# Optimization experiments

Hardware: AMD Instinct MI355X
Metric: run time of the kernel (lower is better)

## Reference

```python
import jax, jax.numpy as jnp
import numpy as np

EMB_DIM = 1024
NUM_HEADS = 16
HEAD_DIM = EMB_DIM // NUM_HEADS  # 64
B, S = 2, 2048


def setup_inputs() -> dict:
    key = jax.random.key(0)
    ks = jax.random.split(key, 9)
    scale = 1.0 / np.sqrt(EMB_DIM)
    return {
        "query": jax.random.normal(ks[0], (B, S, EMB_DIM), dtype=jnp.float32),
        "Wq": jax.random.normal(ks[1], (EMB_DIM, EMB_DIM), dtype=jnp.float32) * scale,
        "bq": jax.random.normal(ks[2], (EMB_DIM,), dtype=jnp.float32) * 0.01,
        "Wk": jax.random.normal(ks[3], (EMB_DIM, EMB_DIM), dtype=jnp.float32) * scale,
        "bk": jax.random.normal(ks[4], (EMB_DIM,), dtype=jnp.float32) * 0.01,
        "Wv": jax.random.normal(ks[5], (EMB_DIM, EMB_DIM), dtype=jnp.float32) * scale,
        "bv": jax.random.normal(ks[6], (EMB_DIM,), dtype=jnp.float32) * 0.01,
        "Wo": jax.random.normal(ks[7], (EMB_DIM, EMB_DIM), dtype=jnp.float32) * scale,
        "bo": jax.random.normal(ks[8], (EMB_DIM,), dtype=jnp.float32) * 0.01,
    }


def reference(query, Wq, bq, Wk, bk, Wv, bv, Wo, bo):
    # Self-attention path (key_value=None, mask=None in the original forward).
    b, s, _ = query.shape
    # torch nn.Linear: y = x @ W.T + b
    def proj(x, W, bias):
        y = jnp.einsum('bse,fe->bsf', x, W) + bias
        # [B,S,E] -> [B,H,S,D]
        return y.reshape(b, s, NUM_HEADS, HEAD_DIM).transpose(0, 2, 1, 3)

    q = proj(query, Wq, bq)
    k = proj(query, Wk, bk)
    v = proj(query, Wv, bv)

    scores = jnp.einsum('bhqd,bhkd->bhqk', q, k) / np.sqrt(HEAD_DIM).astype(np.float32)
    attn = jax.nn.softmax(scores, axis=-1)  # [B,H,S,S]
    out = jnp.einsum('bhqk,bhkd->bhqd', attn, v)
    out = out.transpose(0, 2, 1, 3).reshape(b, s, EMB_DIM)
    return jnp.einsum('bse,fe->bsf', out, Wo) + bo
```

## Files before the change

### kernel.cpp

```cpp
#include <hip/hip_runtime.h>
#include <hip/hip_bf16.h>

using bf16x4 = __attribute__((ext_vector_type(4))) short;
using short8 = __attribute__((ext_vector_type(8))) short;
using f32x4  = __attribute__((ext_vector_type(4))) float;
using f32x16 = __attribute__((ext_vector_type(16))) float;
using u32x2  = __attribute__((ext_vector_type(2))) unsigned;

__device__ __forceinline__ short f2bf(float f) {
  unsigned u = __builtin_bit_cast(unsigned, f);
  u = (u + 0x7fffu + ((u >> 16) & 1u)) >> 16;
  return (short)u;
}
__device__ __forceinline__ unsigned pk2(float a, float b) {
  __hip_bfloat162 h = __float22bfloat162_rn(make_float2(a, b));
  unsigned u; __builtin_memcpy(&u, &h, 4);
  return u;
}
__device__ __forceinline__ void gload16(const short* g, short* l) {
  __builtin_amdgcn_global_load_lds(
      (const __attribute__((address_space(1))) unsigned int*)g,
      (__attribute__((address_space(3))) unsigned int*)l, 16, 0, 0);
}
__device__ __forceinline__ void pl32swap(unsigned &a, unsigned &b) {
  asm("v_permlane32_swap_b32 %0, %1" : "+v"(a), "+v"(b));
}

constexpr int E  = 1024;
constexpr int SL = 2048;
constexpr int NB = 2;
constexpr int NH = 16;
constexpr int M  = NB * SL;

__global__ __launch_bounds__(256) void convert_kernel(
    const float* __restrict__ X,  const float* __restrict__ Wq,
    const float* __restrict__ Wk, const float* __restrict__ Wv,
    const float* __restrict__ Wo, short* __restrict__ out)
{
  const size_t i8 = ((size_t)blockIdx.x * 256 + threadIdx.x) * 8;
  const float* src;
  if (i8 < (size_t)(4u << 20)) {
    src = X + i8;
  } else {
    size_t r = i8 - (size_t)(4u << 20);
    int wi = (int)(r >> 20);
    size_t off = r & ((1u << 20) - 1);
    src = (wi == 0 ? Wq : wi == 1 ? Wk : wi == 2 ? Wv : Wo) + off;
  }
  f32x4 a = *(const f32x4*)src;
  f32x4 b = *(const f32x4*)(src + 4);
  short hb[8];
#pragma unroll
  for (int e = 0; e < 4; ++e) { hb[e] = f2bf(a[e]); hb[4 + e] = f2bf(b[e]); }
  *(short8*)(out + i8) = *(short8*)hb;
}

template <bool OUTF32, bool PROJ>
__device__ __forceinline__ void gemm_body(
    const short* __restrict__ A0, const short* __restrict__ A1, const short* __restrict__ A2,
    const short* __restrict__ B0, const short* __restrict__ B1, const short* __restrict__ B2,
    const float* __restrict__ b0, const float* __restrict__ b1, const float* __restrict__ b2,
    void* __restrict__ Y0, void* __restrict__ Y1, void* __restrict__ Y2,
    float s0, float s1, float s2, int ld0, int ld1, int ld2)
{
  constexpr int BK = 32;
  constexpr int TM = 128, TN = 128;
  constexpr int RA = TM / 64;
  constexpr int RB = TN / 64;
  constexpr int WM = TM / 2, WN = TN / 2;
  constexpr int NI = WM / 16, NJ = WN / 16;
  __shared__ alignas(16) short As[2][TM * BK];
  __shared__ alignas(16) short Bs[2][TN * BK];
  const int t = threadIdx.x;
  const int l = t & 63;
  const int w = t >> 6;
  const int c = l & 15;
  const int g = l >> 4;

  const int fid = (int)blockIdx.x;
  int z, m0, n0;
  if (PROJ) {
    const int orig = (fid & 7) * 96 + (fid >> 3);
    z = orig >> 8;
    const int rem = orig & 255;
    const bool sw = (z != 2);
    m0 = (sw ? (rem >> 5) : (rem & 31)) * TM;
    n0 = (sw ? (rem & 31) : (rem >> 5)) * TN;
  } else {
    const int orig = (fid & 7) * 32 + (fid >> 3);
    z = 0;
    m0 = (orig & 7) * TM;
    n0 = (orig >> 3) * TN;
  }
  const short* Ap = (z == 0) ? A0 : (z == 1) ? A1 : A2;
  const short* Bp = (z == 0) ? B0 : (z == 1) ? B1 : B2;
  const float* bp = (z == 0) ? b0 : (z == 1) ? b1 : b2;
  void* Yp        = (z == 0) ? Y0 : (z == 1) ? Y1 : Y2;
  const float sc  = (z == 0) ? s0 : (z == 1) ? s1 : s2;
  const int ldY   = (z == 0) ? ld0 : (z == 1) ? ld1 : ld2;
  const bool swp  = PROJ ? (z != 2) : true;

  const short* gA[RA]; int oA[RA];
  const short* gB[RB]; int oB[RB];
#pragma unroll
  for (int r = 0; r < RA; ++r) {
    const int cc = r * 256 + t;
    gA[r] = Ap + (size_t)(m0 + (cc >> 2)) * E + (cc & 3) * 8;
    oA[r] = (r * 256 + (t & ~63)) * 8;
  }
#pragma unroll
  for (int r = 0; r < RB; ++r) {
    const int cc = r * 256 + t;
    gB[r] = Bp + (size_t)(n0 + (cc >> 2)) * E + (cc & 3) * 8;
    oB[r] = (r * 256 + (t & ~63)) * 8;
  }

#pragma unroll
  for (int r = 0; r < RA; ++r) gload16(gA[r], &As[0][oA[r]]);
#pragma unroll
  for (int r = 0; r < RB; ++r) gload16(gB[r], &Bs[0][oB[r]]);

  const int wm = (w >> 1) * WM;
  const int wn = (w & 1) * WN;
  f32x4 acc[NI][NJ] = {};
  int cur = 0;

  for (int k0 = 0; k0 < E; k0 += BK) {
    __syncthreads();
    if (k0 + BK < E) {
#pragma unroll
      for (int r = 0; r < RA; ++r) gload16(gA[r] + k0 + BK, &As[cur ^ 1][oA[r]]);
#pragma unroll
      for (int r = 0; r < RB; ++r) gload16(gB[r] + k0 + BK, &Bs[cur ^ 1][oB[r]]);
    }
    short8 ah[NI], bfr[NJ];
#pragma unroll
    for (int i = 0; i < NI; ++i)
      ah[i] = *(const short8*)&As[cur][(wm + i * 16 + c) * BK + g * 8];
#pragma unroll
    for (int j = 0; j < NJ; ++j)
      bfr[j] = *(const short8*)&Bs[cur][(wn + j * 16 + c) * BK + g * 8];
#pragma unroll
    for (int i = 0; i < NI; ++i)
#pragma unroll
      for (int j = 0; j < NJ; ++j)
        acc[i][j] = __builtin_amdgcn_mfma_f32_16x16x32_bf16(ah[i], bfr[j], acc[i][j], 0, 0, 0);
    cur ^= 1;
  }

  float bm[NI][4];
  if (swp) {
#pragma unroll
    for (int i = 0; i < NI; ++i)
#pragma unroll
      for (int r = 0; r < 4; ++r)
        bm[i][r] = bp[m0 + wm + i * 16 + g * 4 + r];
  }
#pragma unroll
  for (int j = 0; j < NJ; ++j) {
    const int col = n0 + wn + j * 16 + c;
    const float bj = swp ? 0.f : bp[col];
#pragma unroll
    for (int i = 0; i < NI; ++i) {
      const int row = m0 + wm + i * 16 + g * 4;
      float v[4];
#pragma unroll
      for (int r = 0; r < 4; ++r)
        v[r] = (acc[i][j][r] + (swp ? bm[i][r] : bj)) * sc;
      if (OUTF32) {
        f32x4 o = {v[0], v[1], v[2], v[3]};
        *(f32x4*)((float*)Yp + (size_t)col * ldY + row) = o;
      } else {
        u32x2 o = {pk2(v[0], v[1]), pk2(v[2], v[3])};
        *(u32x2*)((short*)Yp + (size_t)col * ldY + row) = o;
      }
    }
  }
}

__global__ __launch_bounds__(256) void proj_kernel(
    const short* A0, const short* A1, const short* A2,
    const short* B0, const short* B1, const short* B2,
    const float* b0, const float* b1, const float* b2,
    void* Y0, void* Y1, void* Y2,
    float s0, float s1, float s2, int ld0, int ld1, int ld2)
{
  gemm_body<false, true>(A0, A1, A2, B0, B1, B2, b0, b1, b2,
                         Y0, Y1, Y2, s0, s1, s2, ld0, ld1, ld2);
}

__global__ __launch_bounds__(256) void out_kernel(
    const short* A0, const short* A1, const short* A2,
    const short* B0, const short* B1, const short* B2,
    const float* b0, const float* b1, const float* b2,
    void* Y0, void* Y1, void* Y2,
    float s0, float s1, float s2, int ld0, int ld1, int ld2)
{
  gemm_body<true, false>(A0, A1, A2, B0, B1, B2, b0, b1, b2,
                         Y0, Y1, Y2, s0, s1, s2, ld0, ld1, ld2);
}

__global__ __launch_bounds__(512, 2) void flash_kernel(
    const short* __restrict__ Qm, const short* __restrict__ Km,
    const short* __restrict__ VTm, short* __restrict__ Oh)
{
  __shared__ alignas(16) short Ks[2][64][64];
  __shared__ alignas(16) short Vt[2][64][64];
  const int t = threadIdx.x;
  const int l = t & 63;
  const int w = t >> 6;
  const int c = l & 31;
  const int hi = l >> 5;
  const int fid = (int)blockIdx.x;
  const int orig = (fid & 7) * 32 + (fid >> 3);
  const int q0 = (orig & 7) * 256;
  const int bh = orig >> 3;
  const int bat = bh >> 4;
  const int h = bh & 15;
  const size_t baseK = (size_t)bat * SL * E + h * 64;
  const size_t baseV = (size_t)(h * 64) * M + (size_t)bat * SL;

  short8 qf[4];
  {
    const short* qp = Qm + baseK + (size_t)(q0 + w * 32 + c) * E + hi * 8;
#pragma unroll
    for (int tt = 0; tt < 4; ++tt) qf[tt] = *(const short8*)(qp + tt * 16);
  }

  const int sr = t >> 3, sg = t & 7;
  const int swz = (sg ^ (sr & 7)) * 8;
  const short* gK0 = Km + baseK + (size_t)sr * E + sg * 8;
  const short* gV0 = VTm + baseV + (size_t)sr * M + sg * 8;
  const int wo0 = sr * 64 + swz;

  short8 k0r, v0r;
  k0r = *(const short8*)gK0;
  v0r = *(const short8*)gV0;
  *(short8*)(&Ks[0][0][0] + wo0) = k0r;
  *(short8*)(&Vt[0][0][0] + wo0) = v0r;
  k0r = *(const short8*)(gK0 + (size_t)64 * E);
  v0r = *(const short8*)(gV0 + 64);

  f32x16 oa0 = {}, oa1 = {};
  f32x4 lacc = {0.f, 0.f, 0.f, 0.f};
  __syncthreads();

  constexpr int NTT = SL / 64;
  const int sx = c & 7;
  for (int kt = 0; kt < NTT; ++kt) {
    const int cur = kt & 1;
    if (kt + 1 < NTT) {
      *(short8*)(&Ks[cur ^ 1][0][0] + wo0) = k0r;
      *(short8*)(&Vt[cur ^ 1][0][0] + wo0) = v0r;
      if (kt + 2 < NTT) {
        k0r = *(const short8*)(gK0 + (size_t)(kt + 2) * 64 * E);
        v0r = *(const short8*)(gV0 + (kt + 2) * 64);
      }
    }
    const short* Kc0 = &Ks[cur][c][0];
    const short* Kc1 = &Ks[cur][32 + c][0];
    const short* Vc0 = &Vt[cur][c][0];
    const short* Vc1 = &Vt[cur][32 + c][0];

    f32x16 st0 = {}, st1 = {};
    __builtin_amdgcn_s_setprio(1);
#pragma unroll
    for (int tt = 0; tt < 4; ++tt) {
      const int off = ((tt * 2 + hi) ^ sx) * 8;
      short8 kf0 = *(const short8*)(Kc0 + off);
      short8 kf1 = *(const short8*)(Kc1 + off);
      st0 = __builtin_amdgcn_mfma_f32_32x32x16_bf16(kf0, qf[tt], st0, 0, 0, 0);
      st1 = __builtin_amdgcn_mfma_f32_32x32x16_bf16(kf1, qf[tt], st1, 0, 0, 0);
    }
    __builtin_amdgcn_s_setprio(0);

    float p0[16], p1[16];
#pragma unroll
    for (int i = 0; i < 16; ++i) p0[i] = __builtin_amdgcn_exp2f(st0[i]);
#pragma unroll
    for (int i = 0; i < 16; ++i) p1[i] = __builtin_amdgcn_exp2f(st1[i]);
#pragma unroll
    for (int i = 0; i < 16; ++i) lacc[i & 3] += p0[i] + p1[i];

    unsigned W0[4][2], W1[4][2];
#pragma unroll
    for (int b8 = 0; b8 < 4; ++b8) {
      W0[b8][0] = pk2(p0[4 * b8 + 0], p0[4 * b8 + 1]);
      W0[b8][1] = pk2(p0[4 * b8 + 2], p0[4 * b8 + 3]);
      W1[b8][0] = pk2(p1[4 * b8 + 0], p1[4 * b8 + 1]);
      W1[b8][1] = pk2(p1[4 * b8 + 2], p1[4 * b8 + 3]);
    }

    __builtin_amdgcn_s_setprio(1);
#pragma unroll
    for (int tt = 0; tt < 4; ++tt) {
      unsigned a0, a1, b0, b1;
      if (tt == 0)      { a0 = W0[0][0]; a1 = W0[0][1]; b0 = W0[1][0]; b1 = W0[1][1]; }
      else if (tt == 1) { a0 = W0[2][0]; a1 = W0[2][1]; b0 = W0[3][0]; b1 = W0[3][1]; }
      else if (tt == 2) { a0 = W1[0][0]; a1 = W1[0][1]; b0 = W1[1][0]; b1 = W1[1][1]; }
      else              { a0 = W1[2][0]; a1 = W1[2][1]; b0 = W1[3][0]; b1 = W1[3][1]; }
      pl32swap(a0, b0);
      pl32swap(a1, b1);
      union { unsigned u[4]; short8 s8; } pf;
      pf.u[0] = a0; pf.u[1] = a1; pf.u[2] = b0; pf.u[3] = b1;
      const int off = ((tt * 2 + hi) ^ sx) * 8;
      short8 vf0 = *(const short8*)(Vc0 + off);
      short8 vf1 = *(const short8*)(Vc1 + off);
      oa0 = __builtin_amdgcn_mfma_f32_32x32x16_bf16(vf0, pf.s8, oa0, 0, 0, 0);
      oa1 = __builtin_amdgcn_mfma_f32_32x32x16_bf16(vf1, pf.s8, oa1, 0, 0, 0);
    }
    __builtin_amdgcn_s_setprio(0);
    __syncthreads();
  }

  float s = lacc[0] + lacc[1] + lacc[2] + lacc[3];
  s += __shfl_xor(s, 32);
  const float inv = 1.0f / s;
  const int q = q0 + w * 32 + c;
  short* op = Oh + ((size_t)bat * SL + q) * E + h * 64 + hi * 4;
#pragma unroll
  for (int b8 = 0; b8 < 4; ++b8) {
    u32x2 t0 = {pk2(oa0[4 * b8 + 0] * inv, oa0[4 * b8 + 1] * inv),
                pk2(oa0[4 * b8 + 2] * inv, oa0[4 * b8 + 3] * inv)};
    *(u32x2*)(op + b8 * 8) = t0;
    u32x2 t1 = {pk2(oa1[4 * b8 + 0] * inv, oa1[4 * b8 + 1] * inv),
                pk2(oa1[4 * b8 + 2] * inv, oa1[4 * b8 + 3] * inv)};
    *(u32x2*)(op + 32 + b8 * 8) = t1;
  }
}

extern "C" void kernel_launch(void* const* d_in, const int* in_sizes, int n_in,
                              void* d_out, int out_size, void* d_ws, size_t ws_size,
                              hipStream_t stream)
{
  const float* X  = (const float*)d_in[0];
  const float* Wq = (const float*)d_in[1];
  const float* bq = (const float*)d_in[2];
  const float* Wk = (const float*)d_in[3];
  const float* bk = (const float*)d_in[4];
  const float* Wv = (const float*)d_in[5];
  const float* bv = (const float*)d_in[6];
  const float* Wo = (const float*)d_in[7];
  const float* bo = (const float*)d_in[8];
  float* out = (float*)d_out;

  const size_t szX = (size_t)M * E;
  const size_t szW = (size_t)E * E;
  short* Xb  = (short*)d_ws;
  short* Wqb = Xb + szX;
  short* Wkb = Wqb + szW;
  short* Wvb = Wkb + szW;
  short* Wob = Wvb + szW;
  short* Qw  = Wob + szW;
  short* Kw  = Qw + szX;
  short* VTw = Kw + szX;

  convert_kernel<<<4096, 256, 0, stream>>>(X, Wq, Wk, Wv, Wo, Xb);

  const float kLog2eOver8 = 0.18033688011112042f;
  proj_kernel<<<768, 256, 0, stream>>>(
      Wqb, Wkb, Xb,
      Xb, Xb, Wvb,
      bq, bk, bv,
      (void*)Qw, (void*)Kw, (void*)VTw,
      kLog2eOver8, 1.0f, 1.0f, E, E, M);

  flash_kernel<<<256, 512, 0, stream>>>(Qw, Kw, VTw, Qw );

  out_kernel<<<256, 256, 0, stream>>>(
      Wob, Wob, Wob,
      Qw, Qw, Qw,
      bo, bo, bo,
      (void*)out, (void*)out, (void*)out,
      1.0f, 1.0f, 1.0f, E, E, E);
}
```

Measured before the change: 190.4 us.

## Split-K the output projection GEMM into two halves plus a combine kernel

The output projection GEMM was launched with only 256 blocks, so it splits the K dimension in two, giving 512 blocks that each write a partial fp32 result. One half goes to the output and the other to a scratch buffer aliased onto the K/VT workspace. A new combine kernel then adds the two. This is meant to fill more compute units on the device, at the cost of an extra launch and an extra read-modify-write pass over the 16 MB fp32 output.

```diff
diff --git a/kernel.cpp b/kernel.cpp
--- a/kernel.cpp
+++ b/kernel.cpp
@@ -78,7 +78,9 @@
   const int g = l >> 4;
 
   const int fid = (int)blockIdx.x;
-  int z, m0, n0;
+  int z, m0, n0, kbeg = 0, kend = E;
+  bool biasOn = true;
+  void* Yovr = nullptr;
   if (PROJ) {
     const int orig = (fid & 7) * 96 + (fid >> 3);
     z = orig >> 8;
@@ -87,15 +89,20 @@
     m0 = (sw ? (rem >> 5) : (rem & 31)) * TM;
     n0 = (sw ? (rem & 31) : (rem >> 5)) * TN;
   } else {
-    const int orig = (fid & 7) * 32 + (fid >> 3);
+    const int orig = (fid & 7) * 64 + (fid >> 3);
     z = 0;
-    m0 = (orig & 7) * TM;
-    n0 = (orig >> 3) * TN;
+    const int kh = orig & 1;
+    m0 = ((orig >> 1) & 7) * TM;
+    n0 = (orig >> 4) * TN;
+    kbeg = kh * (E / 2);
+    kend = kbeg + (E / 2);
+    biasOn = (kh == 0);
+    Yovr = kh ? Y1 : Y0;
   }
   const short* Ap = (z == 0) ? A0 : (z == 1) ? A1 : A2;
   const short* Bp = (z == 0) ? B0 : (z == 1) ? B1 : B2;
   const float* bp = (z == 0) ? b0 : (z == 1) ? b1 : b2;
-  void* Yp        = (z == 0) ? Y0 : (z == 1) ? Y1 : Y2;
+  void* Yp        = PROJ ? ((z == 0) ? Y0 : (z == 1) ? Y1 : Y2) : Yovr;
   const float sc  = (z == 0) ? s0 : (z == 1) ? s1 : s2;
   const int ldY   = (z == 0) ? ld0 : (z == 1) ? ld1 : ld2;
   const bool swp  = PROJ ? (z != 2) : true;
@@ -116,18 +123,18 @@
   }
 
 #pragma unroll
-  for (int r = 0; r < RA; ++r) gload16(gA[r], &As[0][oA[r]]);
-#pragma unroll
-  for (int r = 0; r < RB; ++r) gload16(gB[r], &Bs[0][oB[r]]);
+  for (int r = 0; r < RA; ++r) gload16(gA[r] + kbeg, &As[0][oA[r]]);
+#pragma unroll
+  for (int r = 0; r < RB; ++r) gload16(gB[r] + kbeg, &Bs[0][oB[r]]);
 
   const int wm = (w >> 1) * WM;
   const int wn = (w & 1) * WN;
   f32x4 acc[NI][NJ] = {};
   int cur = 0;
 
-  for (int k0 = 0; k0 < E; k0 += BK) {
+  for (int k0 = kbeg; k0 < kend; k0 += BK) {
     __syncthreads();
-    if (k0 + BK < E) {
+    if (k0 + BK < kend) {
 #pragma unroll
       for (int r = 0; r < RA; ++r) gload16(gA[r] + k0 + BK, &As[cur ^ 1][oA[r]]);
 #pragma unroll
@@ -154,12 +161,12 @@
     for (int i = 0; i < NI; ++i)
 #pragma unroll
       for (int r = 0; r < 4; ++r)
-        bm[i][r] = bp[m0 + wm + i * 16 + g * 4 + r];
+        bm[i][r] = biasOn ? bp[m0 + wm + i * 16 + g * 4 + r] : 0.f;
   }
 #pragma unroll
   for (int j = 0; j < NJ; ++j) {
     const int col = n0 + wn + j * 16 + c;
-    const float bj = swp ? 0.f : bp[col];
+    const float bj = (swp || !biasOn) ? 0.f : bp[col];
 #pragma unroll
     for (int i = 0; i < NI; ++i) {
       const int row = m0 + wm + i * 16 + g * 4;
@@ -198,6 +205,17 @@
 {
   gemm_body<true, false>(A0, A1, A2, B0, B1, B2, b0, b1, b2,
                          Y0, Y1, Y2, s0, s1, s2, ld0, ld1, ld2);
+}
+
+__global__ __launch_bounds__(256) void combine_kernel(
+    float* __restrict__ out, const float* __restrict__ p1)
+{
+  const size_t i4 = ((size_t)blockIdx.x * 256 + threadIdx.x) * 4;
+  f32x4 a = *(const f32x4*)(out + i4);
+  f32x4 b = *(const f32x4*)(p1 + i4);
+#pragma unroll
+  for (int e = 0; e < 4; ++e) a[e] += b[e];
+  *(f32x4*)(out + i4) = a;
 }
 
 __global__ __launch_bounds__(512, 2) void flash_kernel(
@@ -354,6 +372,7 @@
   short* Qw  = Wob + szW;
   short* Kw  = Qw + szX;
   short* VTw = Kw + szX;
+  float* P1  = (float*)Kw;
 
   convert_kernel<<<4096, 256, 0, stream>>>(X, Wq, Wk, Wv, Wo, Xb);
 
@@ -367,10 +386,12 @@
 
   flash_kernel<<<256, 512, 0, stream>>>(Qw, Kw, VTw, Qw );
 
-  out_kernel<<<256, 256, 0, stream>>>(
+  out_kernel<<<512, 256, 0, stream>>>(
       Wob, Wob, Wob,
       Qw, Qw, Qw,
       bo, bo, bo,
-      (void*)out, (void*)out, (void*)out,
+      (void*)out, (void*)P1, (void*)out,
       1.0f, 1.0f, 1.0f, E, E, E);
-}
+
+  combine_kernel<<<4096, 256, 0, stream>>>(out, P1);
+}
```

After: 197.8 us. 1.04x slower.
